# Kernel optimization log

Measured on AMD Instinct MI355X. Metric: run time of the kernel, lower is better.

Reference implementation:

```python
import jax, jax.numpy as jnp
import numpy as np

B, C, H, W = 2, 256, 56, 56
NUM_HEADS = 8
K1, K2 = 2, 3
KERNELS = [3, 5, 7]
PADS = [1, 2, 3]
LN_EPS = 1e-5


def setup_inputs() -> dict:
    key = jax.random.key(0)
    ks = jax.random.split(key, 12)
    sc = 1.0 / np.sqrt(C)
    return {
        "x": jax.random.normal(ks[0], (B, C, H, W), jnp.float32),
        "y": jax.random.normal(ks[1], (B, C, H, W), jnp.float32),
        "q_w": jax.random.uniform(ks[2], (C, C), jnp.float32, -sc, sc),
        "q_b": jax.random.uniform(ks[3], (C,), jnp.float32, -sc, sc),
        "kv_w": jax.random.uniform(ks[4], (2 * C, C), jnp.float32, -sc, sc),
        "kv_b": jax.random.uniform(ks[5], (2 * C,), jnp.float32, -sc, sc),
        "proj_w": jax.random.uniform(ks[6], (C, C), jnp.float32, -sc, sc),
        "proj_b": jax.random.uniform(ks[7], (C,), jnp.float32, -sc, sc),
        "ln_w": jnp.ones((C,), jnp.float32),
        "ln_b": jnp.zeros((C,), jnp.float32),
        "attn1_p": jnp.array([0.5], jnp.float32),
        "attn2_p": jnp.array([0.5], jnp.float32),
    }


def _avg_pool(t, k, p):
    # torch AvgPool2d default: divisor is k*k (count_include_pad=True)
    s = jax.lax.reduce_window(t, 0.0, jax.lax.add, (1, 1, k, k), (1, 1, 1, 1),
                              [(0, 0), (0, 0), (p, p), (p, p)])
    return s / float(k * k)


def _topk_masked_softmax(attn, kcount):
    # torch: scatter topk indices into a bool mask, -inf elsewhere, softmax.
    # Equivalent (ties aside, negligible for random floats): threshold at k-th value.
    thr = jax.lax.top_k(attn, kcount)[0][..., -1:]
    return jax.nn.softmax(jnp.where(attn >= thr, attn, -jnp.inf), axis=-1)


def reference(x, y, q_w, q_b, kv_w, kv_b, proj_w, proj_b, ln_w, ln_b, attn1_p, attn2_p):
    h, d = NUM_HEADS, C // NUM_HEADS
    # multiscale pooling (all preserve HxW)
    yp = _avg_pool(y, KERNELS[0], PADS[0]) + _avg_pool(y, KERNELS[1], PADS[1]) + _avg_pool(y, KERNELS[2], PADS[2])
    yf = yp.reshape(B, C, H * W).transpose(0, 2, 1)  # [B, N1, C]
    mu = jnp.mean(yf, -1, keepdims=True)
    var = jnp.var(yf, -1, keepdims=True)
    yf = (yf - mu) / jnp.sqrt(var + LN_EPS) * ln_w + ln_b
    N1 = yf.shape[1]
    kv = (jnp.einsum('bnc,oc->bno', yf, kv_w) + kv_b).reshape(B, N1, 2, h, d)
    kv = kv.transpose(2, 0, 3, 1, 4)  # [2, B, h, N1, d]
    k, v = kv[0], kv[1]
    xf = x.reshape(B, C, H * W).transpose(0, 2, 1)  # [B, N, C]
    q = (jnp.einsum('bnc,oc->bno', xf, q_w) + q_b)
    N = q.shape[1]
    q = q.reshape(B, N, h, d).transpose(0, 2, 1, 3)  # [B, h, N, d]
    attn = jnp.einsum('bhnd,bhmd->bhnm', q, k) * (d ** -0.5)  # [B, h, N, N1]
    a1 = _topk_masked_softmax(attn, max(N1 // K1, 1))
    out1 = jnp.einsum('bhnm,bhmd->bhnd', a1, v)
    a2 = _topk_masked_softmax(attn, max(N1 // K2, 1))
    out2 = jnp.einsum('bhnm,bhmd->bhnd', a2, v)
    out = out1 * attn1_p + out2 * attn2_p
    out = out.transpose(0, 2, 1, 3).reshape(B, N, C)
    out = jnp.einsum('bnc,oc->bno', out, proj_w) + proj_b
    hw = int(N ** 0.5)
    return out.transpose(0, 2, 1).reshape(B, C, hw, hw)
```

## Files before the change

kernel.cpp:

```cpp
#include <hip/hip_runtime.h>

#define B_    2
#define C_    256
#define HW_   56
#define N_    3136
#define NH_   8
#define D_    32
#define K1CNT 1568
#define K2CNT 1045
#define LN_EPS 1e-5f
#define SROW  3140
#define ROWS  4
#define PROBS 8
#define HISTW 4096
#define CAP   896
#define RM    8.0f


__device__ inline unsigned ordf(float f) {
    unsigned u = __float_as_uint(f);
    return u ^ (((unsigned)((int)u >> 31)) | 0x80000000u);
}

__device__ inline float redsum64(float v) {
    v += __int_as_float(__builtin_amdgcn_ds_swizzle(__float_as_int(v), 0x041F));
    v += __int_as_float(__builtin_amdgcn_ds_swizzle(__float_as_int(v), 0x081F));
    v += __int_as_float(__builtin_amdgcn_ds_swizzle(__float_as_int(v), 0x101F));
    v += __int_as_float(__builtin_amdgcn_ds_swizzle(__float_as_int(v), 0x201F));
    v += __int_as_float(__builtin_amdgcn_ds_swizzle(__float_as_int(v), 0x401F));
    v += __shfl_xor(v, 32, 64);
    return v;
}

__device__ inline float avred(float v) {
    v += __int_as_float(__builtin_amdgcn_ds_swizzle(__float_as_int(v), 0x201F));
    v += __int_as_float(__builtin_amdgcn_ds_swizzle(__float_as_int(v), 0x401F));
    v += __shfl_xor(v, 32, 64);
    return v;
}

__global__ void pool_kernel(const float* __restrict__ y, float* __restrict__ yp)
{
    int gid = blockIdx.x * 256 + threadIdx.x;
    int n  = gid % N_;
    int bc = gid / N_;
    const float* src = y + (size_t)bc * N_;
    int x0 = n % HW_, y0 = n / HW_;
    float acc = 0.f;
#pragma unroll
    for (int dy = -3; dy <= 3; ++dy) {
        int yy = y0 + dy;
        if ((unsigned)yy >= HW_) continue;
#pragma unroll
        for (int dx = -3; dx <= 3; ++dx) {
            int xx = x0 + dx;
            if ((unsigned)xx >= HW_) continue;
            float w = 1.f / 49.f;
            if (dy >= -2 && dy <= 2 && dx >= -2 && dx <= 2) w += 1.f / 25.f;
            if (dy >= -1 && dy <= 1 && dx >= -1 && dx <= 1) w += 1.f / 9.f;
            acc += w * src[yy * HW_ + xx];
        }
    }
    yp[gid] = acc;
}

__global__ void ln_kernel(const float* __restrict__ yp, const float* __restrict__ lnw,
                          const float* __restrict__ lnb, float* __restrict__ yfT)
{
    __shared__ float wr[8];
    __shared__ float stats[2];
    int idx = blockIdx.x;
    int b = idx / N_, n = idx % N_;
    int c = threadIdx.x;
    size_t off = ((size_t)b * C_ + c) * N_ + n;
    float v = yp[off];
    float s = v, q = v * v;
    int lane = threadIdx.x & 63, wid = threadIdx.x >> 6;
#pragma unroll
    for (int d = 32; d; d >>= 1) { s += __shfl_down(s, d, 64); q += __shfl_down(q, d, 64); }
    if (lane == 0) { wr[wid] = s; wr[4 + wid] = q; }
    __syncthreads();
    if (threadIdx.x == 0) {
        float ts = wr[0] + wr[1] + wr[2] + wr[3];
        float tq = wr[4] + wr[5] + wr[6] + wr[7];
        float mu = ts * (1.f / C_);
        float var = tq * (1.f / C_) - mu * mu;
        stats[0] = mu; stats[1] = rsqrtf(var + LN_EPS);
    }
    __syncthreads();
    yfT[off] = (v - stats[0]) * stats[1] * lnw[c] + lnb[c];
}

__global__ __launch_bounds__(256) void gemm_qkv(
    const float* __restrict__ A, const float* __restrict__ W,
    const float* __restrict__ bias, float* __restrict__ dst0,
    float* __restrict__ dst1, float scale)
{
    __shared__ float As[16][64];
    __shared__ float Ws[16][68];
    int tid = threadIdx.x;
    int m0 = blockIdx.x * 64;
    int b = m0 / N_, n0 = m0 % N_;
    int o0 = blockIdx.y * 64;
    const float* Ab = A + (size_t)b * C_ * N_;
    float acc[4][4] = {};
    int la_k = tid >> 4;
    int la_m = (tid & 15) * 4;
    int lw_o = tid >> 2;
    int lw_k = (tid & 3) * 4;
    int u  = tid & 15;
    int v_ = tid >> 4;
    for (int kt = 0; kt < 16; ++kt) {
        int k0 = kt * 16;
        float4 av = *(const float4*)&Ab[(size_t)(k0 + la_k) * N_ + n0 + la_m];
        float4 wv = *(const float4*)&W[(size_t)(o0 + lw_o) * C_ + k0 + lw_k];
        __syncthreads();
        *(float4*)&As[la_k][la_m] = av;
        Ws[lw_k + 0][lw_o] = wv.x; Ws[lw_k + 1][lw_o] = wv.y;
        Ws[lw_k + 2][lw_o] = wv.z; Ws[lw_k + 3][lw_o] = wv.w;
        __syncthreads();
#pragma unroll
        for (int k = 0; k < 16; ++k) {
            float4 wf = *(const float4*)&Ws[k][u * 4];
            float a0 = As[k][v_], a1 = As[k][v_ + 16], a2 = As[k][v_ + 32], a3 = As[k][v_ + 48];
            acc[0][0] += wf.x * a0; acc[0][1] += wf.x * a1; acc[0][2] += wf.x * a2; acc[0][3] += wf.x * a3;
            acc[1][0] += wf.y * a0; acc[1][1] += wf.y * a1; acc[1][2] += wf.y * a2; acc[1][3] += wf.y * a3;
            acc[2][0] += wf.z * a0; acc[2][1] += wf.z * a1; acc[2][2] += wf.z * a2; acc[2][3] += wf.z * a3;
            acc[3][0] += wf.w * a0; acc[3][1] += wf.w * a1; acc[3][2] += wf.w * a2; acc[3][3] += wf.w * a3;
        }
    }
    int oc = o0 + u * 4;
    float b0v = bias[oc], b1v = bias[oc + 1], b2v = bias[oc + 2], b3v = bias[oc + 3];
    float* dst = dst0; int c2 = oc;
    if (dst1 && oc >= C_) { dst = dst1; c2 = oc - C_; }
    int h = c2 >> 5, d0 = c2 & 31;
    size_t base = ((size_t)b * NH_ + h) * N_ * D_;
#pragma unroll
    for (int j = 0; j < 4; ++j) {
        int n = n0 + v_ + j * 16;
        float4 val;
        val.x = (acc[0][j] + b0v) * scale;
        val.y = (acc[1][j] + b1v) * scale;
        val.z = (acc[2][j] + b2v) * scale;
        val.w = (acc[3][j] + b3v) * scale;
        *(float4*)&dst[base + (size_t)n * D_ + d0] = val;
    }
}

__global__ __launch_bounds__(256) void gemm_proj(
    const float* __restrict__ A, const float* __restrict__ W,
    const float* __restrict__ bias, float* __restrict__ out)
{
    __shared__ float As[16][64];
    __shared__ float Ws[16][68];
    int tid = threadIdx.x;
    int m0 = blockIdx.x * 64;
    int b = m0 / N_, n0 = m0 % N_;
    int o0 = blockIdx.y * 64;
    const float* Ab = A + (size_t)b * C_ * N_;
    float acc[4][4] = {};
    int la_k = tid >> 4;
    int la_m = (tid & 15) * 4;
    int lw_o = tid >> 2;
    int lw_k = (tid & 3) * 4;
    int u  = tid & 15;
    int v_ = tid >> 4;
    for (int kt = 0; kt < 16; ++kt) {
        int k0 = kt * 16;
        float4 av = *(const float4*)&Ab[(size_t)(k0 + la_k) * N_ + n0 + la_m];
        float4 wv = *(const float4*)&W[(size_t)(o0 + lw_o) * C_ + k0 + lw_k];
        __syncthreads();
        *(float4*)&As[la_k][la_m] = av;
        Ws[lw_k + 0][lw_o] = wv.x; Ws[lw_k + 1][lw_o] = wv.y;
        Ws[lw_k + 2][lw_o] = wv.z; Ws[lw_k + 3][lw_o] = wv.w;
        __syncthreads();
#pragma unroll
        for (int k = 0; k < 16; ++k) {
            float4 af = *(const float4*)&As[k][u * 4];
            float w0 = Ws[k][v_], w1 = Ws[k][v_ + 16], w2 = Ws[k][v_ + 32], w3 = Ws[k][v_ + 48];
            acc[0][0] += w0 * af.x; acc[0][1] += w0 * af.y; acc[0][2] += w0 * af.z; acc[0][3] += w0 * af.w;
            acc[1][0] += w1 * af.x; acc[1][1] += w1 * af.y; acc[1][2] += w1 * af.z; acc[1][3] += w1 * af.w;
            acc[2][0] += w2 * af.x; acc[2][1] += w2 * af.y; acc[2][2] += w2 * af.z; acc[2][3] += w2 * af.w;
            acc[3][0] += w3 * af.x; acc[3][1] += w3 * af.y; acc[3][2] += w3 * af.z; acc[3][3] += w3 * af.w;
        }
    }
#pragma unroll
    for (int i = 0; i < 4; ++i) {
        int o = o0 + v_ + i * 16;
        float bb = bias[o];
        float4 val;
        val.x = acc[i][0] + bb; val.y = acc[i][1] + bb;
        val.z = acc[i][2] + bb; val.w = acc[i][3] + bb;
        *(float4*)&out[((size_t)b * C_ + o) * N_ + n0 + u * 4] = val;
    }
}

struct AttnMisc {
    unsigned thrBin[PROBS];
    int selrM[PROBS];
    unsigned thrU[PROBS];
    unsigned cntM[PROBS];
    float coef[PROBS];
    float pp[2];
    float wred[32];
};

#define REFINE_BSUM(NV)                                                    \
    {                                                                      \
        unsigned vv[NV]; unsigned aok = 0;                                 \
        _Pragma("unroll")                                                  \
        for (int t = 0; t < NV; ++t) {                                     \
            int idx = lane + (t << 6);                                     \
            bool ok = idx < cnt;                                           \
            vv[t] = ok ? cp[idx] : 0u;                                     \
            if (ok) aok |= 1u << t;                                        \
        }                                                                  \
        unsigned act = aok;                                                \
        for (int b = 20; b >= 0; --b) {                                    \
            unsigned msk = 0, c = 0;                                       \
            _Pragma("unroll")                                              \
            for (int t = 0; t < NV; ++t) {                                 \
                bool p = ((act >> t) & 1u) && ((vv[t] >> b) & 1u);         \
                c += (unsigned)__popcll(__ballot(p));                      \
                if (p) msk |= 1u << t;                                     \
            }                                                              \
            if (c >= kk) { act = msk; bits |= 1u << b; }                   \
            else { kk -= c; act &= ~msk; }                                 \
        }                                                                  \
        unsigned thr = (bin << 21) | bits;                                 \
        _Pragma("unroll")                                                  \
        for (int t = 0; t < NV; ++t) {                                     \
            if (((aok >> t) & 1u) && vv[t] >= thr) {                       \
                unsigned uo = vv[t] ^ (~((unsigned)((int)vv[t] >> 31)) | 0x80000000u); \
                bsum += __expf(__uint_as_float(uo) - RM);                  \
            }                                                              \
        }                                                                  \
    }

__global__ __launch_bounds__(1024, 8) void attn_kernel(
    const float* __restrict__ qh, const float* __restrict__ kh, const float* __restrict__ vh,
    const float* __restrict__ p1p, const float* __restrict__ p2p,
    float* __restrict__ aoT)
{
    extern __shared__ char smem[];
    float*    S    = (float*)smem;
    unsigned* hist = (unsigned*)(smem + 50240);
    unsigned* cand = (unsigned*)(smem + 50240);
    float*    red  = (float*)(smem + 50240);
    AttnMisc* M    = (AttnMisc*)(smem + 50240 + 28672);

    int tid = threadIdx.x, lane = tid & 63, wid = tid >> 6;
    int bh = blockIdx.y, n0 = blockIdx.x * ROWS;
    size_t bhN = (size_t)bh * N_;

    if (tid < PROBS) M->cntM[tid] = 0u;
    if (tid == 0) { M->pp[0] = p1p[0]; M->pp[1] = p2p[0]; }
    for (int i = tid; i < HISTW; i += 1024) hist[i] = 0u;
    __syncthreads();

    const float* qrow = qh + (bhN + n0) * D_;
    for (int i = 0; i < 4; ++i) {
        int j = tid + (i << 10);
        if (j < N_) {
            const float4* kp = (const float4*)(kh + (bhN + j) * D_);
            float4 k4[8];
#pragma unroll
            for (int q = 0; q < 8; ++q) k4[q] = kp[q];
#pragma unroll
            for (int r = 0; r < ROWS; ++r) {
                const float4* qp = (const float4*)(qrow + r * D_);
                float s = 0.f;
#pragma unroll
                for (int q = 0; q < 8; ++q) {
                    float4 q4 = qp[q];
                    s += q4.x * k4[q].x + q4.y * k4[q].y + q4.z * k4[q].z + q4.w * k4[q].w;
                }
                S[r * SROW + j] = s;
                unsigned bin = ordf(s) >> 21;
                atomicAdd(&hist[(r << 10) + (bin >> 1)], 1u << ((bin & 1) << 4));
            }
        }
    }
    __syncthreads();

    if (wid < PROBS) {
        int prob = wid;
        int r = prob >> 1;
        int k = (prob & 1) ? K2CNT : K1CNT;
        const unsigned* hrow = hist + (r << 10) + (lane << 4);
        uint4 ha = *(const uint4*)(hrow + 0);
        uint4 hb = *(const uint4*)(hrow + 4);
        uint4 hc = *(const uint4*)(hrow + 8);
        uint4 hd = *(const uint4*)(hrow + 12);
        unsigned hh[16] = { ha.x, ha.y, ha.z, ha.w, hb.x, hb.y, hb.z, hb.w,
                            hc.x, hc.y, hc.z, hc.w, hd.x, hd.y, hd.z, hd.w };
        unsigned usum = 0;
#pragma unroll
        for (int t = 0; t < 16; ++t) usum += hh[t];
        int ltot = (int)((usum & 0xFFFFu) + (usum >> 16));
        int s = ltot;
#pragma unroll
        for (int d = 1; d < 64; d <<= 1) {
            int o = __shfl_down(s, d, 64);
            if (lane + d < 64) s += o;
        }
        int after = s - ltot;
        if (after < k && after + ltot >= k) {
            int g = after, b0 = -1, selr = 0;
#pragma unroll
            for (int m = 31; m >= 0; --m) {
                unsigned w = hh[m >> 1];
                int cm = (m & 1) ? (int)(w >> 16) : (int)(w & 0xFFFFu);
                g += cm;
                if (b0 < 0 && g >= k) { b0 = (lane << 5) + m; selr = k - (g - cm); }
            }
            M->thrBin[prob] = (unsigned)b0;
            M->selrM[prob] = selr;
        }
    }
    __syncthreads();

    {
        int row = wid >> 2;
        int sub = ((wid & 3) << 6) | lane;
        unsigned tb1 = M->thrBin[2 * row], tb2 = M->thrBin[2 * row + 1];
        int p1 = 2 * row, p2 = 2 * row + 1;
        float ds1 = 0.f, ds2 = 0.f;
        const float* Srow = S + row * SROW;
#pragma unroll
        for (int i = 0; i < 4; ++i) {
            int q = sub + (i << 8);
            if (q < 784) {
                float4 sv = *(const float4*)&Srow[q << 2];
                float sa[4] = { sv.x, sv.y, sv.z, sv.w };
#pragma unroll
                for (int t = 0; t < 4; ++t) {
                    unsigned u = ordf(sa[t]);
                    unsigned bin = u >> 21;
                    if (bin > tb1) {
                        float w = __expf(sa[t] - RM);
                        ds1 += w;
                        if (bin > tb2) ds2 += w;
                    }
                    if (bin == tb1) {
                        unsigned ix = atomicAdd(&M->cntM[p1], 1u);
                        if (ix < CAP) cand[p1 * CAP + ix] = u;
                    }
                    if (bin == tb2) {
                        unsigned ix = atomicAdd(&M->cntM[p2], 1u);
                        if (ix < CAP) cand[p2 * CAP + ix] = u;
                    }
                }
            }
        }
        ds1 = redsum64(ds1);
        ds2 = redsum64(ds2);
        if (lane == 0) { M->wred[wid * 2] = ds1; M->wred[wid * 2 + 1] = ds2; }
    }
    __syncthreads();

    if (wid < PROBS) {
        int prob = wid;
        int cnt = (int)M->cntM[prob]; if (cnt > CAP) cnt = CAP;
        unsigned kk = (unsigned)M->selrM[prob];
        unsigned bin = M->thrBin[prob];
        const unsigned* cp = cand + prob * CAP;
        unsigned bits = 0;
        float bsum = 0.f;
        if (cnt <= 64)       REFINE_BSUM(1)
        else if (cnt <= 192) REFINE_BSUM(3)
        else                 REFINE_BSUM(15)
        bsum = redsum64(bsum);
        if (lane == 0) {
            M->thrU[prob] = (bin << 21) | bits;
            int rw = (prob >> 1) << 2;
            float denom = bsum
                + M->wred[(rw + 0) * 2 + (prob & 1)]
                + M->wred[(rw + 1) * 2 + (prob & 1)]
                + M->wred[(rw + 2) * 2 + (prob & 1)]
                + M->wred[(rw + 3) * 2 + (prob & 1)];
            M->coef[prob] = M->pp[prob & 1] / denom;
        }
    }
    __syncthreads();

    {
        int row = wid >> 2;
        int sub = ((wid & 3) << 6) | lane;
        unsigned u1 = M->thrU[2 * row], u2 = M->thrU[2 * row + 1];
        float c1 = M->coef[2 * row];
        float c12 = c1 + M->coef[2 * row + 1];
        float* Srow = S + row * SROW;
#pragma unroll
        for (int i = 0; i < 4; ++i) {
            int q = sub + (i << 8);
            if (q < 784) {
                float4 sv = *(const float4*)&Srow[q << 2];
                float sa[4] = { sv.x, sv.y, sv.z, sv.w };
#pragma unroll
                for (int t = 0; t < 4; ++t) {
                    float a = sa[t];
                    unsigned u = ordf(a);
                    float c = 0.f;
                    if (u >= u1) {
                        float w = __expf(a - RM);
                        c = (u >= u2) ? w * c12 : w * c1;
                    }
                    sa[t] = c;
                }
                *(float4*)&Srow[q << 2] = make_float4(sa[0], sa[1], sa[2], sa[3]);
            }
        }
    }
    __syncthreads();

    int jj4 = lane >> 3, dq = lane & 7;
    float4 acc[ROWS];
#pragma unroll
    for (int r = 0; r < ROWS; ++r) acc[r] = make_float4(0.f, 0.f, 0.f, 0.f);
    const float* vbase = vh + bhN * D_ + (dq << 2);
    for (int g = wid; g < 98; g += 16) {
        int jb = (g << 5) + (jj4 << 2);
        float4 v0 = *(const float4*)(vbase + (size_t)(jb + 0) * D_);
        float4 v1 = *(const float4*)(vbase + (size_t)(jb + 1) * D_);
        float4 v2 = *(const float4*)(vbase + (size_t)(jb + 2) * D_);
        float4 v3 = *(const float4*)(vbase + (size_t)(jb + 3) * D_);
#pragma unroll
        for (int r = 0; r < ROWS; ++r) {
            float4 s4 = *(const float4*)&S[r * SROW + jb];
            acc[r].x += s4.x * v0.x + s4.y * v1.x + s4.z * v2.x + s4.w * v3.x;
            acc[r].y += s4.x * v0.y + s4.y * v1.y + s4.z * v2.y + s4.w * v3.y;
            acc[r].z += s4.x * v0.z + s4.y * v1.z + s4.z * v2.z + s4.w * v3.z;
            acc[r].w += s4.x * v0.w + s4.y * v1.w + s4.z * v2.w + s4.w * v3.w;
        }
    }
#pragma unroll
    for (int r = 0; r < ROWS; ++r) {
        acc[r].x = avred(acc[r].x);
        acc[r].y = avred(acc[r].y);
        acc[r].z = avred(acc[r].z);
        acc[r].w = avred(acc[r].w);
    }
    if (lane < 8) {
#pragma unroll
        for (int r = 0; r < ROWS; ++r)
            *(float4*)&red[(wid << 7) + (r << 5) + (lane << 2)] = acc[r];
    }
    __syncthreads();
    if (tid < 32 * ROWS) {
        float o = 0.f;
#pragma unroll
        for (int w = 0; w < 16; ++w) o += red[(w << 7) + tid];
        int r = tid >> 5, d = tid & 31;
        int b = bh >> 3, h = bh & 7;
        aoT[((size_t)(b * C_ + h * 32 + d)) * N_ + n0 + r] = o;
    }
}

static const int ATTN_SMEM = 50240 + 28672 + (int)sizeof(AttnMisc);

extern "C" void kernel_launch(void* const* d_in, const int* in_sizes, int n_in,
                              void* d_out, int out_size, void* d_ws, size_t ws_size,
                              hipStream_t stream)
{
    (void)in_sizes; (void)n_in; (void)out_size; (void)ws_size;
    const float* x    = (const float*)d_in[0];
    const float* y    = (const float*)d_in[1];
    const float* q_w  = (const float*)d_in[2];
    const float* q_b  = (const float*)d_in[3];
    const float* kv_w = (const float*)d_in[4];
    const float* kv_b = (const float*)d_in[5];
    const float* p_w  = (const float*)d_in[6];
    const float* p_b  = (const float*)d_in[7];
    const float* lnw  = (const float*)d_in[8];
    const float* lnb  = (const float*)d_in[9];
    const float* a1p  = (const float*)d_in[10];
    const float* a2p  = (const float*)d_in[11];
    float* out = (float*)d_out;

    float* ws = (float*)d_ws;
    const size_t PLANE = (size_t)B_ * C_ * N_;
    float* yp  = ws;
    float* yfT = ws + PLANE;
    float* qh_ = ws + 2 * PLANE;
    float* kh_ = ws + 3 * PLANE;
    float* vh_ = ws + 4 * PLANE;
    float* aoT = ws + 5 * PLANE;

    pool_kernel<<<dim3((unsigned)(PLANE / 256)), 256, 0, stream>>>(y, yp);
    ln_kernel<<<dim3(B_ * N_), 256, 0, stream>>>(yp, lnw, lnb, yfT);
    gemm_qkv<<<dim3(98, 4), 256, 0, stream>>>(x, q_w, q_b, qh_, nullptr, 0.17677669529663687f);
    gemm_qkv<<<dim3(98, 8), 256, 0, stream>>>(yfT, kv_w, kv_b, kh_, vh_, 1.0f);
    hipFuncSetAttribute(reinterpret_cast<const void*>(attn_kernel),
                        hipFuncAttributeMaxDynamicSharedMemorySize, ATTN_SMEM);
    attn_kernel<<<dim3(N_ / ROWS, B_ * NH_), 1024, ATTN_SMEM, stream>>>(qh_, kh_, vh_, a1p, a2p, aoT);
    gemm_proj<<<dim3(98, 4), 256, 0, stream>>>(aoT, p_w, p_b, out);
}
```

Before: 1.013 ms.

## Select top-k on precomputed exp weights with a narrower histogram

```diff
diff --git a/kernel.cpp b/kernel.cpp
--- a/kernel.cpp
+++ b/kernel.cpp
@@ -12,15 +12,12 @@
 #define SROW  3140
 #define ROWS  4
 #define PROBS 8
-#define HISTW 4096
-#define CAP   896
+#define NBIN  1024
+#define WBASE 14336
+#define HISTW 2048
+#define CAP   256
 #define RM    8.0f
 
-
-__device__ inline unsigned ordf(float f) {
-    unsigned u = __float_as_uint(f);
-    return u ^ (((unsigned)((int)u >> 31)) | 0x80000000u);
-}
 
 __device__ inline float redsum64(float v) {
     v += __int_as_float(__builtin_amdgcn_ds_swizzle(__float_as_int(v), 0x041F));
@@ -216,7 +213,7 @@
             if (ok) aok |= 1u << t;                                        \
         }                                                                  \
         unsigned act = aok;                                                \
-        for (int b = 20; b >= 0; --b) {                                    \
+        for (int b = 15; b >= 0; --b) {                                    \
             unsigned msk = 0, c = 0;                                       \
             _Pragma("unroll")                                              \
             for (int t = 0; t < NV; ++t) {                                 \
@@ -227,13 +224,11 @@
             if (c >= kk) { act = msk; bits |= 1u << b; }                   \
             else { kk -= c; act &= ~msk; }                                 \
         }                                                                  \
-        unsigned thr = (bin << 21) | bits;                                 \
+        unsigned thr = lo | bits;                                          \
         _Pragma("unroll")                                                  \
         for (int t = 0; t < NV; ++t) {                                     \
-            if (((aok >> t) & 1u) && vv[t] >= thr) {                       \
-                unsigned uo = vv[t] ^ (~((unsigned)((int)vv[t] >> 31)) | 0x80000000u); \
-                bsum += __expf(__uint_as_float(uo) - RM);                  \
-            }                                                              \
+            if (((aok >> t) & 1u) && vv[t] >= thr)                         \
+                bsum += __uint_as_float(vv[t]);                            \
         }                                                                  \
     }
 
@@ -247,7 +242,7 @@
     unsigned* hist = (unsigned*)(smem + 50240);
     unsigned* cand = (unsigned*)(smem + 50240);
     float*    red  = (float*)(smem + 50240);
-    AttnMisc* M    = (AttnMisc*)(smem + 50240 + 28672);
+    AttnMisc* M    = (AttnMisc*)(smem + 50240 + 8192);
 
     int tid = threadIdx.x, lane = tid & 63, wid = tid >> 6;
     int bh = blockIdx.y, n0 = blockIdx.x * ROWS;
@@ -255,7 +250,8 @@
 
     if (tid < PROBS) M->cntM[tid] = 0u;
     if (tid == 0) { M->pp[0] = p1p[0]; M->pp[1] = p2p[0]; }
-    for (int i = tid; i < HISTW; i += 1024) hist[i] = 0u;
+    if (tid < HISTW) hist[tid] = 0u;
+    if (tid + 1024 < HISTW) hist[tid + 1024] = 0u;
     __syncthreads();
 
     const float* qrow = qh + (bhN + n0) * D_;
@@ -275,9 +271,11 @@
                     float4 q4 = qp[q];
                     s += q4.x * k4[q].x + q4.y * k4[q].y + q4.z * k4[q].z + q4.w * k4[q].w;
                 }
-                S[r * SROW + j] = s;
-                unsigned bin = ordf(s) >> 21;
-                atomicAdd(&hist[(r << 10) + (bin >> 1)], 1u << ((bin & 1) << 4));
+                float w = __expf(s - RM);
+                S[r * SROW + j] = w;
+                int bin = (int)(__float_as_uint(w) >> 16) - WBASE;
+                bin = max(0, min(bin, NBIN - 1));
+                atomicAdd(&hist[(r << 9) + (bin >> 1)], 1u << ((bin & 1) << 4));
             }
         }
     }
@@ -287,16 +285,13 @@
         int prob = wid;
         int r = prob >> 1;
         int k = (prob & 1) ? K2CNT : K1CNT;
-        const unsigned* hrow = hist + (r << 10) + (lane << 4);
+        const unsigned* hrow = hist + (r << 9) + (lane << 3);
         uint4 ha = *(const uint4*)(hrow + 0);
         uint4 hb = *(const uint4*)(hrow + 4);
-        uint4 hc = *(const uint4*)(hrow + 8);
-        uint4 hd = *(const uint4*)(hrow + 12);
-        unsigned hh[16] = { ha.x, ha.y, ha.z, ha.w, hb.x, hb.y, hb.z, hb.w,
-                            hc.x, hc.y, hc.z, hc.w, hd.x, hd.y, hd.z, hd.w };
+        unsigned hh[8] = { ha.x, ha.y, ha.z, ha.w, hb.x, hb.y, hb.z, hb.w };
         unsigned usum = 0;
 #pragma unroll
-        for (int t = 0; t < 16; ++t) usum += hh[t];
+        for (int t = 0; t < 8; ++t) usum += hh[t];
         int ltot = (int)((usum & 0xFFFFu) + (usum >> 16));
         int s = ltot;
 #pragma unroll
@@ -308,11 +303,11 @@
         if (after < k && after + ltot >= k) {
             int g = after, b0 = -1, selr = 0;
 #pragma unroll
-            for (int m = 31; m >= 0; --m) {
+            for (int m = 15; m >= 0; --m) {
                 unsigned w = hh[m >> 1];
                 int cm = (m & 1) ? (int)(w >> 16) : (int)(w & 0xFFFFu);
                 g += cm;
-                if (b0 < 0 && g >= k) { b0 = (lane << 5) + m; selr = k - (g - cm); }
+                if (b0 < 0 && g >= k) { b0 = (lane << 4) + m; selr = k - (g - cm); }
             }
             M->thrBin[prob] = (unsigned)b0;
             M->selrM[prob] = selr;
@@ -323,7 +318,8 @@
     {
         int row = wid >> 2;
         int sub = ((wid & 3) << 6) | lane;
-        unsigned tb1 = M->thrBin[2 * row], tb2 = M->thrBin[2 * row + 1];
+        unsigned lo1 = (unsigned)(WBASE + M->thrBin[2 * row]) << 16, hi1 = lo1 + 0x10000u;
+        unsigned lo2 = (unsigned)(WBASE + M->thrBin[2 * row + 1]) << 16, hi2 = lo2 + 0x10000u;
         int p1 = 2 * row, p2 = 2 * row + 1;
         float ds1 = 0.f, ds2 = 0.f;
         const float* Srow = S + row * SROW;
@@ -335,18 +331,15 @@
                 float sa[4] = { sv.x, sv.y, sv.z, sv.w };
 #pragma unroll
                 for (int t = 0; t < 4; ++t) {
-                    unsigned u = ordf(sa[t]);
-                    unsigned bin = u >> 21;
-                    if (bin > tb1) {
-                        float w = __expf(sa[t] - RM);
-                        ds1 += w;
-                        if (bin > tb2) ds2 += w;
-                    }
-                    if (bin == tb1) {
+                    unsigned u = __float_as_uint(sa[t]);
+                    if (u >= hi1) {
+                        ds1 += sa[t];
+                        if (u >= hi2) ds2 += sa[t];
+                    } else if (u >= lo1) {
                         unsigned ix = atomicAdd(&M->cntM[p1], 1u);
                         if (ix < CAP) cand[p1 * CAP + ix] = u;
                     }
-                    if (bin == tb2) {
+                    if (u >= lo2 && u < hi2) {
                         unsigned ix = atomicAdd(&M->cntM[p2], 1u);
                         if (ix < CAP) cand[p2 * CAP + ix] = u;
                     }
@@ -363,16 +356,16 @@
         int prob = wid;
         int cnt = (int)M->cntM[prob]; if (cnt > CAP) cnt = CAP;
         unsigned kk = (unsigned)M->selrM[prob];
-        unsigned bin = M->thrBin[prob];
+        unsigned lo = (unsigned)(WBASE + M->thrBin[prob]) << 16;
         const unsigned* cp = cand + prob * CAP;
         unsigned bits = 0;
         float bsum = 0.f;
         if (cnt <= 64)       REFINE_BSUM(1)
-        else if (cnt <= 192) REFINE_BSUM(3)
-        else                 REFINE_BSUM(15)
+        else if (cnt <= 128) REFINE_BSUM(2)
+        else                 REFINE_BSUM(4)
         bsum = redsum64(bsum);
         if (lane == 0) {
-            M->thrU[prob] = (bin << 21) | bits;
+            M->thrU[prob] = lo | bits;
             int rw = (prob >> 1) << 2;
             float denom = bsum
                 + M->wred[(rw + 0) * 2 + (prob & 1)]
@@ -399,14 +392,9 @@
                 float sa[4] = { sv.x, sv.y, sv.z, sv.w };
 #pragma unroll
                 for (int t = 0; t < 4; ++t) {
-                    float a = sa[t];
-                    unsigned u = ordf(a);
-                    float c = 0.f;
-                    if (u >= u1) {
-                        float w = __expf(a - RM);
-                        c = (u >= u2) ? w * c12 : w * c1;
-                    }
-                    sa[t] = c;
+                    unsigned u = __float_as_uint(sa[t]);
+                    float sel = (u >= u2) ? c12 : c1;
+                    sa[t] = (u >= u1) ? sa[t] * sel : 0.f;
                 }
                 *(float4*)&Srow[q << 2] = make_float4(sa[0], sa[1], sa[2], sa[3]);
             }
@@ -457,7 +445,7 @@
     }
 }
 
-static const int ATTN_SMEM = 50240 + 28672 + (int)sizeof(AttnMisc);
+static const int ATTN_SMEM = 50240 + 8192 + (int)sizeof(AttnMisc);
 
 extern "C" void kernel_launch(void* const* d_in, const int* in_sizes, int n_in,
                               void* d_out, int out_size, void* d_ws, size_t ws_size,
```

Result: faster. 943.3 us (-6.8%).
